# Kernel optimization log

Hardware: AMD Instinct MI355X
Metric: run time of the kernel (lower is better)

The kernel has to match this reference:

```python
import jax, jax.numpy as jnp
import numpy as np

KERNEL_MUL = 2.0
KERNEL_NUM = 5
EPS = 1e-06
CLAMP_MAX = 50.0


def setup_inputs() -> dict:
    key = jax.random.key(0)
    k1, k2 = jax.random.split(key)
    B, D = 2048, 2048
    source = jax.random.normal(k1, (B, D), dtype=jnp.float32)
    target = jax.random.normal(k2, (B, D), dtype=jnp.float32)
    return {"source": source, "target": target}


def _mmd_rbf(source, target):
    B = source.shape[0]
    total = jnp.concatenate([source, target], axis=0)  # [2B, D]
    total = jnp.nan_to_num(total, nan=0.0, posinf=10000.0, neginf=-10000.0)
    # squared pairwise distances via |a|^2 + |b|^2 - 2 a.b (same math as (diff**2).sum(-1))
    sq = jnp.sum(total * total, axis=1)                       # [2B]
    L2 = sq[:, None] + sq[None, :] - 2.0 * (total @ total.T)  # [2B, 2B]
    L2 = jnp.maximum(L2, 0.0)
    # bandwidth: detached mean of L2, clamped
    bw = jax.lax.stop_gradient(jnp.maximum(jnp.mean(L2), EPS))
    kernels = jnp.zeros_like(L2)
    for i in range(KERNEL_NUM):
        bw_i = jnp.maximum(bw * (KERNEL_MUL ** i), EPS)
        scaled = jnp.minimum(L2 / bw_i, CLAMP_MAX)
        kernels = kernels + jnp.exp(-scaled)
    XX = jnp.mean(kernels[:B, :B])
    YY = jnp.mean(kernels[B:, B:])
    XY = jnp.mean(kernels[:B, B:])
    YX = jnp.mean(kernels[B:, :B])
    loss = XX + YY - XY - YX
    # auto_fallback: linear MMD (detached) if RBF loss is non-finite
    delta = jnp.mean(source, axis=0) - jnp.mean(target, axis=0)
    lin = jax.lax.stop_gradient(jnp.dot(delta, delta))
    return jnp.where(jnp.isfinite(loss), loss, lin)


def reference(source, target):
    return _mmd_rbf(source, target)
```

## Files before the change

### kernel.cpp

```cpp
#include <hip/hip_runtime.h>
#include <cstdint>
#include <cmath>

#define DD 2048
#define NROW 4096
#define BHALF 2048
#define NT 16

typedef __attribute__((ext_vector_type(4))) int i32x4;
typedef __attribute__((ext_vector_type(8))) signed char c8;

typedef __attribute__((address_space(1))) const void* as1cv;
typedef __attribute__((address_space(3))) void* as3v;

__device__ __forceinline__ void gload_lds16(const void* g, void* l) {
  __builtin_amdgcn_global_load_lds((as1cv)g, (as3v)l, 16, 0, 0);
}

__device__ __forceinline__ float fixv(float x) {
  if (isnan(x)) return 0.0f;
  if (isinf(x)) return x > 0.0f ? 10000.0f : -10000.0f;
  return x;
}

constexpr size_t TQ_OFF     = 0;
constexpr size_t SQ8_OFF    = (size_t)NROW * DD;
constexpr size_t CS_SRC_OFF = SQ8_OFF + NROW * 4;
constexpr size_t CS_TGT_OFF = CS_SRC_OFF + DD * 4;
constexpr size_t ACC_OFF    = CS_TGT_OFF + DD * 4;
constexpr size_t SCAL_OFF   = ACC_OFF + 4 * 8;
constexpr size_t CNT_OFF    = SCAL_OFF + 8;
constexpr size_t ZERO_BYTES = 16384 + 8192 + 8192 + 32 + 8 + 8;

__global__ __launch_bounds__(512) void k_prep(const float* __restrict__ src,
                                              const float* __restrict__ tgt,
                                              signed char* __restrict__ Tq,
                                              int* __restrict__ sq8,
                                              float* __restrict__ cs_src,
                                              float* __restrict__ cs_tgt) {
  int b = blockIdx.x;
  int rb = b >> 4, cb = b & 15;
  int t = threadIdx.x;
  int cl = t & 15;
  int rt = t >> 4;
  const float* base;
  float* csp;
  if (rb < 8) { base = src + (size_t)(rb * 256) * DD; csp = cs_src; }
  else        { base = tgt + (size_t)(rb - 8) * 256 * DD; csp = cs_tgt; }
  int c0 = cb * 128 + cl * 8;
  float cacc[8] = {0, 0, 0, 0, 0, 0, 0, 0};
  __shared__ float cpart[32][16][8];
#pragma unroll
  for (int pass = 0; pass < 8; ++pass) {
    int row = pass * 32 + rt;
    const float4* p = (const float4*)(base + (size_t)row * DD + c0);
    float4 v0 = p[0], v1 = p[1];
    float x[8] = {v0.x, v0.y, v0.z, v0.w, v1.x, v1.y, v1.z, v1.w};
    c8 qq;
    int a = 0;
#pragma unroll
    for (int j = 0; j < 8; ++j) {
      float f = fixv(x[j]);
      int qi = __float2int_rn(f * 16.0f);
      qi = max(-127, min(127, qi));
      a += qi * qi;
      cacc[j] += (float)qi;
      qq[j] = (signed char)qi;
    }
    *(c8*)(Tq + (size_t)(rb * 256 + row) * DD + c0) = qq;
    a += __shfl_xor(a, 1); a += __shfl_xor(a, 2);
    a += __shfl_xor(a, 4); a += __shfl_xor(a, 8);
    if (cl == 0) atomicAdd(&sq8[rb * 256 + row], a);
  }
#pragma unroll
  for (int j = 0; j < 8; ++j) cpart[rt][cl][j] = cacc[j];
  __syncthreads();
  if (t < 128) {
    int cl2 = t >> 3, j = t & 7;
    float s = 0.0f;
#pragma unroll
    for (int r2 = 0; r2 < 32; ++r2) s += cpart[r2][cl2][j];
    atomicAdd(&csp[cb * 128 + cl2 * 8 + j], s);
  }
}

__global__ __launch_bounds__(512, 2) void k_mmd(const signed char* __restrict__ Tq,
                                                const int* __restrict__ sq8,
                                                const float* __restrict__ cs_src,
                                                const float* __restrict__ cs_tgt,
                                                double* __restrict__ accd,
                                                float* __restrict__ scal,
                                                unsigned int* __restrict__ cnt,
                                                float* __restrict__ out) {
  int lin = blockIdx.x;
  int t5 = (lin & 7) * 32 + (lin >> 3);
  int bi = t5 >> 4, bj = t5 & 15;

  __shared__ __attribute__((aligned(16))) signed char Sb[131072];

  int tid = threadIdx.x, l = tid & 63, w = tid >> 6;
  int wr = w >> 2, wc = w & 3;
  int l15 = l & 15;

  i32x4 acc[8][4];
#pragma unroll
  for (int m = 0; m < 8; ++m)
#pragma unroll
    for (int n = 0; n < 4; ++n) acc[m][n] = (i32x4){0, 0, 0, 0};

  int colsw = ((l & 3) ^ ((l >> 3) & 3)) * 16;
  size_t gA0 = (size_t)(bi * 256 + w * 16 + (l >> 2)) * DD + colsw;
  size_t gB0 = (size_t)(bj * 256 + w * 16 + (l >> 2)) * DD + colsw;
  int dW = w * 1024;

#define CALLA(bf, kc, h, T) gload_lds16(                                        \
      Tq + gA0 + (size_t)(h) * 128 * DD + (size_t)(T) * 128 + (kc) * 64,        \
      (void*)(Sb + (bf) + (kc) * 32768 + (h) * 8192 + dW))
#define CALLB(bf, kc, h, T) gload_lds16(                                        \
      Tq + gB0 + (size_t)(h) * 128 * DD + (size_t)(T) * 128 + (kc) * 64,        \
      (void*)(Sb + (bf) + (kc) * 32768 + 16384 + (h) * 8192 + dW))

  int slotx = (((l >> 4) ^ ((l15 >> 1) & 3))) * 16;
  int aB = (wr * 128 + l15) * 64 + slotx;
  int bB = 16384 + (wc * 64 + l15) * 64 + slotx;

#define BAR()  __builtin_amdgcn_s_barrier()
#define LGKM0() asm volatile("s_waitcnt lgkmcnt(0)" ::: "memory")

#pragma unroll
  for (int kc = 0; kc < 2; ++kc)
#pragma unroll
    for (int h = 0; h < 2; ++h) { CALLA(0, kc, h, 0); CALLB(0, kc, h, 0); }
  asm volatile("s_waitcnt vmcnt(0)" ::: "memory");
  BAR();

#pragma unroll 1
  for (int t = 0; t < NT; ++t) {
    const int bf = (t & 1) << 16;
    const int ob = bf ^ 65536;
    i32x4 aF[4][2], bF[4][2];
#pragma unroll
    for (int kc = 0; kc < 2; ++kc) {
#pragma unroll
      for (int mi = 0; mi < 4; ++mi)
        aF[mi][kc] = *(const i32x4*)(Sb + bf + kc * 32768 + aB + mi * 1024);
#pragma unroll
      for (int n = 0; n < 4; ++n)
        bF[n][kc] = *(const i32x4*)(Sb + bf + kc * 32768 + bB + n * 1024);
    }
    if (t < NT - 1) {
#pragma unroll
      for (int kc = 0; kc < 2; ++kc)
#pragma unroll
        for (int h = 0; h < 2; ++h) { CALLA(ob, kc, h, t + 1); CALLB(ob, kc, h, t + 1); }
    }
    BAR();
    LGKM0();
    __builtin_amdgcn_s_setprio(1);
#pragma unroll
    for (int mi = 0; mi < 4; ++mi)
#pragma unroll
      for (int n = 0; n < 4; ++n)
#pragma unroll
        for (int kc = 0; kc < 2; ++kc)
          acc[mi][n] = __builtin_amdgcn_mfma_i32_16x16x64_i8(aF[mi][kc], bF[n][kc], acc[mi][n], 0, 0, 0);
    __builtin_amdgcn_s_setprio(0);
    BAR();
    i32x4 aG[4][2];
#pragma unroll
    for (int kc = 0; kc < 2; ++kc)
#pragma unroll
      for (int mi = 0; mi < 4; ++mi)
        aG[mi][kc] = *(const i32x4*)(Sb + bf + kc * 32768 + aB + (4 + mi) * 1024);
    LGKM0();
    __builtin_amdgcn_s_setprio(1);
#pragma unroll
    for (int mi = 0; mi < 4; ++mi)
#pragma unroll
      for (int n = 0; n < 4; ++n)
#pragma unroll
        for (int kc = 0; kc < 2; ++kc)
          acc[4 + mi][n] = __builtin_amdgcn_mfma_i32_16x16x64_i8(aG[mi][kc], bF[n][kc], acc[4 + mi][n], 0, 0, 0);
    __builtin_amdgcn_s_setprio(0);
    if (t < NT - 1) asm volatile("s_waitcnt vmcnt(0)" ::: "memory");
    BAR();
  }

  float* red = (float*)Sb;
  float bw;
  {
    float ssq = 0.0f, s2 = 0.0f, dl = 0.0f;
#pragma unroll
    for (int k2 = 0; k2 < 8; ++k2) ssq += (float)sq8[tid + k2 * 512];
#pragma unroll
    for (int k2 = 0; k2 < 4; ++k2) {
      int c = tid + k2 * 512;
      float a = cs_src[c], b2 = cs_tgt[c];
      float s = a + b2;
      s2 += s * s;
      float d = a - b2;
      dl += d * d;
    }
    for (int o = 32; o; o >>= 1) {
      ssq += __shfl_xor(ssq, o);
      s2  += __shfl_xor(s2, o);
      dl  += __shfl_xor(dl, o);
    }
    __syncthreads();
    if (l == 0) { red[w] = ssq; red[8 + w] = s2; red[16 + w] = dl; }
    __syncthreads();
    double S = 0.0, Q = 0.0;
#pragma unroll
    for (int i = 0; i < 8; ++i) { S += red[i]; Q += red[8 + i]; }
    double meanL2 = (2.0 * S / (double)NROW -
                     2.0 * Q / ((double)NROW * (double)NROW)) * (1.0 / 256.0);
    bw = (float)fmax(meanL2, 1e-6);
    if (tid == 0 && lin == 0) {
      double L = 0.0;
      for (int i = 0; i < 8; ++i) L += red[16 + i];
      scal[0] = (float)(L * (1.0 / (256.0 * 4194304.0)));
    }
  }

  float inv4 = 1.0f / fmaxf(bw * 16.0f, 1e-6f);

  float sum = 0.0f;
  int rbase = bi * 256 + wr * 128 + ((l >> 4) * 4);
  int cbase = bj * 256 + wc * 64 + l15;
#pragma unroll
  for (int m = 0; m < 8; ++m) {
    int4 sr = *(const int4*)(sq8 + rbase + m * 16);
    int sqr[4] = {sr.x, sr.y, sr.z, sr.w};
#pragma unroll
    for (int n = 0; n < 4; ++n) {
      int sc = sq8[cbase + n * 16];
#pragma unroll
      for (int r = 0; r < 4; ++r) {
        float L2 = (float)(sqr[r] + sc - 2 * acc[m][n][r]) * (1.0f / 256.0f);
        L2 = fmaxf(L2, 0.0f);
        float e4 = __expf(-L2 * inv4);
        float e3 = e4 * e4;
        float e2 = e3 * e3;
        float e1 = e2 * e2;
        float e0 = e1 * e1;
        sum += ((e0 + e1) + (e2 + e3)) + e4;
      }
    }
  }
  for (int o = 32; o; o >>= 1) sum += __shfl_xor(sum, o);
  if (l == 0) red[32 + w] = sum;
  __syncthreads();
  if (tid == 0) {
    double tot = 0.0;
    for (int i = 0; i < 8; ++i) tot += red[32 + i];
    int cat = (bi >= 8) * 2 + (bj >= 8);
    atomicAdd(accd + cat, tot);
    __threadfence();
    unsigned int old = atomicAdd(cnt, 1u);
    if (old == 255u) {
      __threadfence();
      double loss = (accd[0] + accd[3] - accd[1] - accd[2]) * (1.0 / 4194304.0);
      if (!isfinite(loss)) loss = (double)scal[0];
      out[0] = (float)loss;
    }
  }
}

extern "C" void kernel_launch(void* const* d_in, const int* in_sizes, int n_in,
                              void* d_out, int out_size, void* d_ws, size_t ws_size,
                              hipStream_t stream) {
  const float* src = (const float*)d_in[0];
  const float* tgt = (const float*)d_in[1];
  char* ws = (char*)d_ws;
  signed char* Tq  = (signed char*)(ws + TQ_OFF);
  int*    sq8    = (int*)(ws + SQ8_OFF);
  float*  cs_src = (float*)(ws + CS_SRC_OFF);
  float*  cs_tgt = (float*)(ws + CS_TGT_OFF);
  double* accd   = (double*)(ws + ACC_OFF);
  float*  scal   = (float*)(ws + SCAL_OFF);
  unsigned int* cnt = (unsigned int*)(ws + CNT_OFF);

  hipMemsetAsync(ws + SQ8_OFF, 0, ZERO_BYTES, stream);

  k_prep<<<256, 512, 0, stream>>>(src, tgt, Tq, sq8, cs_src, cs_tgt);
  k_mmd<<<256, 512, 0, stream>>>(Tq, sq8, cs_src, cs_tgt, accd, scal, cnt,
                                 (float*)d_out);
}
```

Before: 66.81 us.

## Switch int8 GEMM to 32x32x32 MFMA tiles and split prep into smaller blocks

The main GEMM loop now uses 32x32x32 int8 MFMA instructions with 16-element accumulators instead of 16x16x64. The LDS fragment addressing and the epilogue's row/column mapping are rebuilt to match the new output layout. The goal is fewer LDS fragment reads per MFMA and better operand reuse per instruction. The prep kernel is relaunched as 512 blocks of 256 threads covering 128 rows each, to raise parallelism. The risks are LDS bank conflicts under the new swizzle and more register pressure from the larger accumulators.

```diff
diff --git a/kernel.cpp b/kernel.cpp
--- a/kernel.cpp
+++ b/kernel.cpp
@@ -8,6 +8,7 @@
 #define NT 16
 
 typedef __attribute__((ext_vector_type(4))) int i32x4;
+typedef __attribute__((ext_vector_type(16))) int i32x16;
 typedef __attribute__((ext_vector_type(8))) signed char c8;
 
 typedef __attribute__((address_space(1))) const void* as1cv;
@@ -32,7 +33,7 @@
 constexpr size_t CNT_OFF    = SCAL_OFF + 8;
 constexpr size_t ZERO_BYTES = 16384 + 8192 + 8192 + 32 + 8 + 8;
 
-__global__ __launch_bounds__(512) void k_prep(const float* __restrict__ src,
+__global__ __launch_bounds__(256) void k_prep(const float* __restrict__ src,
                                               const float* __restrict__ tgt,
                                               signed char* __restrict__ Tq,
                                               int* __restrict__ sq8,
@@ -45,14 +46,14 @@
   int rt = t >> 4;
   const float* base;
   float* csp;
-  if (rb < 8) { base = src + (size_t)(rb * 256) * DD; csp = cs_src; }
-  else        { base = tgt + (size_t)(rb - 8) * 256 * DD; csp = cs_tgt; }
+  if (rb < 16) { base = src + (size_t)(rb * 128) * DD; csp = cs_src; }
+  else         { base = tgt + (size_t)(rb - 16) * 128 * DD; csp = cs_tgt; }
   int c0 = cb * 128 + cl * 8;
   float cacc[8] = {0, 0, 0, 0, 0, 0, 0, 0};
-  __shared__ float cpart[32][16][8];
+  __shared__ float cpart[16][16][8];
 #pragma unroll
   for (int pass = 0; pass < 8; ++pass) {
-    int row = pass * 32 + rt;
+    int row = pass * 16 + rt;
     const float4* p = (const float4*)(base + (size_t)row * DD + c0);
     float4 v0 = p[0], v1 = p[1];
     float x[8] = {v0.x, v0.y, v0.z, v0.w, v1.x, v1.y, v1.z, v1.w};
@@ -67,10 +68,10 @@
       cacc[j] += (float)qi;
       qq[j] = (signed char)qi;
     }
-    *(c8*)(Tq + (size_t)(rb * 256 + row) * DD + c0) = qq;
+    *(c8*)(Tq + (size_t)(rb * 128 + row) * DD + c0) = qq;
     a += __shfl_xor(a, 1); a += __shfl_xor(a, 2);
     a += __shfl_xor(a, 4); a += __shfl_xor(a, 8);
-    if (cl == 0) atomicAdd(&sq8[rb * 256 + row], a);
+    if (cl == 0) atomicAdd(&sq8[rb * 128 + row], a);
   }
 #pragma unroll
   for (int j = 0; j < 8; ++j) cpart[rt][cl][j] = cacc[j];
@@ -79,7 +80,7 @@
     int cl2 = t >> 3, j = t & 7;
     float s = 0.0f;
 #pragma unroll
-    for (int r2 = 0; r2 < 32; ++r2) s += cpart[r2][cl2][j];
+    for (int r2 = 0; r2 < 16; ++r2) s += cpart[r2][cl2][j];
     atomicAdd(&csp[cb * 128 + cl2 * 8 + j], s);
   }
 }
@@ -100,13 +101,15 @@
 
   int tid = threadIdx.x, l = tid & 63, w = tid >> 6;
   int wr = w >> 2, wc = w & 3;
-  int l15 = l & 15;
-
-  i32x4 acc[8][4];
-#pragma unroll
-  for (int m = 0; m < 8; ++m)
-#pragma unroll
-    for (int n = 0; n < 4; ++n) acc[m][n] = (i32x4){0, 0, 0, 0};
+  int l31 = l & 31;
+
+  i32x16 acc[4][2];
+#pragma unroll
+  for (int m = 0; m < 4; ++m)
+#pragma unroll
+    for (int n = 0; n < 2; ++n)
+#pragma unroll
+      for (int e = 0; e < 16; ++e) acc[m][n][e] = 0;
 
   int colsw = ((l & 3) ^ ((l >> 3) & 3)) * 16;
   size_t gA0 = (size_t)(bi * 256 + w * 16 + (l >> 2)) * DD + colsw;
@@ -120,9 +123,15 @@
       Tq + gB0 + (size_t)(h) * 128 * DD + (size_t)(T) * 128 + (kc) * 64,        \
       (void*)(Sb + (bf) + (kc) * 32768 + 16384 + (h) * 8192 + dW))
 
-  int slotx = (((l >> 4) ^ ((l15 >> 1) & 3))) * 16;
-  int aB = (wr * 128 + l15) * 64 + slotx;
-  int bB = 16384 + (wc * 64 + l15) * 64 + slotx;
+  int fsw = (l >> 1) & 3;
+  int p16[4];
+  p16[0] = (((l >> 5) + 0) ^ fsw) * 16;
+  p16[1] = (((l >> 5) + 2) ^ fsw) * 16;
+  int aRow = (wr * 128 + l31) * 64;
+  int bRow = 16384 + (wc * 64 + l31) * 64;
+
+#define ARD(bf, mi, ks) (*(const i32x4*)(Sb + (bf) + ((ks) >> 1) * 32768 + aRow + (mi) * 2048 + p16[(ks) & 1]))
+#define BRD(bf, ni, ks) (*(const i32x4*)(Sb + (bf) + ((ks) >> 1) * 32768 + bRow + (ni) * 2048 + p16[(ks) & 1]))
 
 #define BAR()  __builtin_amdgcn_s_barrier()
 #define LGKM0() asm volatile("s_waitcnt lgkmcnt(0)" ::: "memory")
@@ -138,15 +147,13 @@
   for (int t = 0; t < NT; ++t) {
     const int bf = (t & 1) << 16;
     const int ob = bf ^ 65536;
-    i32x4 aF[4][2], bF[4][2];
-#pragma unroll
-    for (int kc = 0; kc < 2; ++kc) {
-#pragma unroll
-      for (int mi = 0; mi < 4; ++mi)
-        aF[mi][kc] = *(const i32x4*)(Sb + bf + kc * 32768 + aB + mi * 1024);
-#pragma unroll
-      for (int n = 0; n < 4; ++n)
-        bF[n][kc] = *(const i32x4*)(Sb + bf + kc * 32768 + bB + n * 1024);
+    i32x4 aF[2][4], bF[2][4];
+#pragma unroll
+    for (int ks = 0; ks < 4; ++ks) {
+#pragma unroll
+      for (int mi = 0; mi < 2; ++mi) aF[mi][ks] = ARD(bf, mi, ks);
+#pragma unroll
+      for (int ni = 0; ni < 2; ++ni) bF[ni][ks] = BRD(bf, ni, ks);
     }
     if (t < NT - 1) {
 #pragma unroll
@@ -158,29 +165,28 @@
     LGKM0();
     __builtin_amdgcn_s_setprio(1);
 #pragma unroll
-    for (int mi = 0; mi < 4; ++mi)
-#pragma unroll
-      for (int n = 0; n < 4; ++n)
-#pragma unroll
-        for (int kc = 0; kc < 2; ++kc)
-          acc[mi][n] = __builtin_amdgcn_mfma_i32_16x16x64_i8(aF[mi][kc], bF[n][kc], acc[mi][n], 0, 0, 0);
+    for (int mi = 0; mi < 2; ++mi)
+#pragma unroll
+      for (int ni = 0; ni < 2; ++ni)
+#pragma unroll
+        for (int ks = 0; ks < 4; ++ks)
+          acc[mi][ni] = __builtin_amdgcn_mfma_i32_32x32x32_i8(aF[mi][ks], bF[ni][ks], acc[mi][ni], 0, 0, 0);
     __builtin_amdgcn_s_setprio(0);
     BAR();
-    i32x4 aG[4][2];
-#pragma unroll
-    for (int kc = 0; kc < 2; ++kc)
-#pragma unroll
-      for (int mi = 0; mi < 4; ++mi)
-        aG[mi][kc] = *(const i32x4*)(Sb + bf + kc * 32768 + aB + (4 + mi) * 1024);
+    i32x4 aG[2][4];
+#pragma unroll
+    for (int ks = 0; ks < 4; ++ks)
+#pragma unroll
+      for (int mi = 0; mi < 2; ++mi) aG[mi][ks] = ARD(bf, 2 + mi, ks);
     LGKM0();
     __builtin_amdgcn_s_setprio(1);
 #pragma unroll
-    for (int mi = 0; mi < 4; ++mi)
-#pragma unroll
-      for (int n = 0; n < 4; ++n)
-#pragma unroll
-        for (int kc = 0; kc < 2; ++kc)
-          acc[4 + mi][n] = __builtin_amdgcn_mfma_i32_16x16x64_i8(aG[mi][kc], bF[n][kc], acc[4 + mi][n], 0, 0, 0);
+    for (int mi = 0; mi < 2; ++mi)
+#pragma unroll
+      for (int ni = 0; ni < 2; ++ni)
+#pragma unroll
+        for (int ks = 0; ks < 4; ++ks)
+          acc[2 + mi][ni] = __builtin_amdgcn_mfma_i32_32x32x32_i8(aG[mi][ks], bF[ni][ks], acc[2 + mi][ni], 0, 0, 0);
     __builtin_amdgcn_s_setprio(0);
     if (t < NT - 1) asm volatile("s_waitcnt vmcnt(0)" ::: "memory");
     BAR();
@@ -225,25 +231,28 @@
   float inv4 = 1.0f / fmaxf(bw * 16.0f, 1e-6f);
 
   float sum = 0.0f;
-  int rbase = bi * 256 + wr * 128 + ((l >> 4) * 4);
-  int cbase = bj * 256 + wc * 64 + l15;
-#pragma unroll
-  for (int m = 0; m < 8; ++m) {
-    int4 sr = *(const int4*)(sq8 + rbase + m * 16);
-    int sqr[4] = {sr.x, sr.y, sr.z, sr.w};
-#pragma unroll
-    for (int n = 0; n < 4; ++n) {
-      int sc = sq8[cbase + n * 16];
-#pragma unroll
-      for (int r = 0; r < 4; ++r) {
-        float L2 = (float)(sqr[r] + sc - 2 * acc[m][n][r]) * (1.0f / 256.0f);
-        L2 = fmaxf(L2, 0.0f);
-        float e4 = __expf(-L2 * inv4);
-        float e3 = e4 * e4;
-        float e2 = e3 * e3;
-        float e1 = e2 * e2;
-        float e0 = e1 * e1;
-        sum += ((e0 + e1) + (e2 + e3)) + e4;
+  int rbase = bi * 256 + wr * 128 + 4 * (l >> 5);
+  int cbase = bj * 256 + wc * 64 + l31;
+#pragma unroll
+  for (int mi = 0; mi < 4; ++mi) {
+#pragma unroll
+    for (int g = 0; g < 4; ++g) {
+      int4 sr = *(const int4*)(sq8 + rbase + mi * 32 + g * 8);
+      int sqr[4] = {sr.x, sr.y, sr.z, sr.w};
+#pragma unroll
+      for (int ni = 0; ni < 2; ++ni) {
+        int sc = sq8[cbase + ni * 32];
+#pragma unroll
+        for (int q = 0; q < 4; ++q) {
+          float L2 = (float)(sqr[q] + sc - 2 * acc[mi][ni][4 * g + q]) * (1.0f / 256.0f);
+          L2 = fmaxf(L2, 0.0f);
+          float e4 = __expf(-L2 * inv4);
+          float e3 = e4 * e4;
+          float e2 = e3 * e3;
+          float e1 = e2 * e2;
+          float e0 = e1 * e1;
+          sum += ((e0 + e1) + (e2 + e3)) + e4;
+        }
       }
     }
   }
@@ -282,7 +291,7 @@
 
   hipMemsetAsync(ws + SQ8_OFF, 0, ZERO_BYTES, stream);
 
-  k_prep<<<256, 512, 0, stream>>>(src, tgt, Tq, sq8, cs_src, cs_tgt);
+  k_prep<<<512, 256, 0, stream>>>(src, tgt, Tq, sq8, cs_src, cs_tgt);
   k_mmd<<<256, 512, 0, stream>>>(Tq, sq8, cs_src, cs_tgt, accd, scal, cnt,
                                  (float*)d_out);
 }
```

After: 68.09 us. No clear change (+1.9%).
